# Optimization experiments

Hardware: AMD Instinct MI355X
Metric: run time of the kernel (lower is better)

The kernel has to match this reference:

```python
import jax, jax.numpy as jnp
import numpy as np
import math

B, T, C, NH = 4, 2048, 1024, 16
HS = C // NH  # 64

def rope_cache(dim, max_pos):
    half = dim // 2
    inv_freq = 1.0 / (10000.0 ** (jnp.arange(half, dtype=jnp.float32) * 2.0 / dim))
    ang = jnp.arange(max_pos, dtype=jnp.float32)[:, None] * inv_freq[None, :]
    return jnp.cos(ang), jnp.sin(ang)  # each [T, half]

def apply_rope(x, cos, sin):
    # x: [B, nH, T, hs]; rotate consecutive pairs (complex multiply)
    x0 = x[..., 0::2]
    x1 = x[..., 1::2]
    c = cos[None, None, :, :]
    s = sin[None, None, :, :]
    r0 = x0 * c - x1 * s
    r1 = x0 * s + x1 * c
    return jnp.stack([r0, r1], axis=-1).reshape(x.shape)

def setup_inputs() -> dict:
    key = jax.random.key(0)
    ks = jax.random.split(key, 5)
    sc = 1.0 / math.sqrt(C)
    return {
        "x": jax.random.normal(ks[0], (B, T, C), jnp.float32),
        "Wq": jax.random.normal(ks[1], (C, C), jnp.float32) * sc,
        "bq": jnp.zeros((C,), jnp.float32),
        "Wk": jax.random.normal(ks[2], (C, C), jnp.float32) * sc,
        "bk": jnp.zeros((C,), jnp.float32),
        "Wv": jax.random.normal(ks[3], (C, C), jnp.float32) * sc,
        "bv": jnp.zeros((C,), jnp.float32),
        "Wp": jax.random.normal(ks[4], (C, C), jnp.float32) * sc,
        "bp": jnp.zeros((C,), jnp.float32),
    }

def reference(x, Wq, bq, Wk, bk, Wv, bv, Wp, bp):
    Bx, Tx, Cx = x.shape
    def split_heads(y):
        return y.reshape(Bx, Tx, NH, HS).transpose(0, 2, 1, 3)  # [B,nH,T,hs]
    q = split_heads(x @ Wq + bq)
    k = split_heads(x @ Wk + bk)
    v = split_heads(x @ Wv + bv)
    cos, sin = rope_cache(HS, Tx)
    q = apply_rope(q, cos, sin)
    k = apply_rope(k, cos, sin)
    att = jnp.einsum("bhqd,bhkd->bhqk", q, k) * (1.0 / math.sqrt(HS))
    causal = jnp.tril(jnp.ones((Tx, Tx), bool))
    att = jnp.where(causal[None, None, :, :], att, jnp.float32(-1e10))
    att = jax.nn.softmax(att, axis=-1)
    y = jnp.einsum("bhqk,bhkd->bhqd", att, v)
    y = y.transpose(0, 2, 1, 3).reshape(Bx, Tx, Cx)
    return y @ Wp + bp
```

## Files before the change

kernel.cpp:

```cpp
#include <hip/hip_runtime.h>
#include <math.h>

#define B_  4
#define T_  2048
#define C_  1024
#define NH_ 16
#define HS_ 64
#define M_  (B_ * T_)
#define BH_ (B_ * NH_)

typedef __bf16 bf16_t;
typedef __bf16 bf16x8 __attribute__((ext_vector_type(8)));
typedef float  f32x4  __attribute__((ext_vector_type(4)));

__device__ __forceinline__ f32x4 mfma16(bf16x8 a, bf16x8 b, f32x4 c) {
    return __builtin_amdgcn_mfma_f32_16x16x32_bf16(a, b, c, 0, 0, 0);
}

#define GLOAD16(gp, lp) __builtin_amdgcn_global_load_lds( \
    (const __attribute__((address_space(1))) void*)(gp),  \
    (__attribute__((address_space(3))) void*)(lp), 16, 0, 0)


__global__ void cvt_x(const float* __restrict__ x, bf16_t* __restrict__ xb) {
    int i = blockIdx.x * blockDim.x + threadIdx.x;
    const float4* src = reinterpret_cast<const float4*>(x);
    float4 u = src[2 * i], v = src[2 * i + 1];
    bf16x8 o;
    o[0] = (bf16_t)u.x; o[1] = (bf16_t)u.y; o[2] = (bf16_t)u.z; o[3] = (bf16_t)u.w;
    o[4] = (bf16_t)v.x; o[5] = (bf16_t)v.y; o[6] = (bf16_t)v.z; o[7] = (bf16_t)v.w;
    *reinterpret_cast<bf16x8*>(xb + (size_t)i * 8) = o;
}

__global__ void wtrans(const float* __restrict__ W, bf16_t* __restrict__ Wt) {
    __shared__ float tile[32][33];
    int bx = blockIdx.x, by = blockIdx.y;
    int tx = threadIdx.x, ty = threadIdx.y;
    #pragma unroll
    for (int j = 0; j < 4; ++j)
        tile[ty + j * 8][tx] = W[(size_t)(by * 32 + ty + j * 8) * 1024 + bx * 32 + tx];
    __syncthreads();
    #pragma unroll
    for (int j = 0; j < 4; ++j)
        Wt[(size_t)(bx * 32 + ty + j * 8) * 1024 + by * 32 + tx] = (bf16_t)tile[tx][ty + j * 8];
}

__global__ void rope_tab(float* __restrict__ cs, float* __restrict__ sn) {
    int idx = blockIdx.x * blockDim.x + threadIdx.x;
    int t = idx >> 5, j = idx & 31;
    float inv = 1.0f / powf(10000.0f, ((float)(2 * j)) / 64.0f);
    float ang = (float)t * inv;
    cs[idx] = cosf(ang);
    sn[idx] = sinf(ang);
}

__global__ __launch_bounds__(512) void gemm_qkv(
    const bf16_t* __restrict__ A, const bf16_t* __restrict__ Bt,
    const float* __restrict__ bq, const float* __restrict__ bk, const float* __restrict__ bv,
    bf16_t* __restrict__ outq, bf16_t* __restrict__ outk, bf16_t* __restrict__ outvt) {
    __shared__ __align__(16) bf16_t Ab[2][256 * 64];
    __shared__ __align__(16) bf16_t Bb[2][128 * 64];
    int tid = threadIdx.x;
    int lane = tid & 63, w = tid >> 6;
    int rr = lane & 15, g = lane >> 4;
    int lin = blockIdx.y * 24 + blockIdx.x;
    int swz = (lin & 7) * 96 + (lin >> 3);
    int bx = swz % 24, by = swz / 24;
    int mbase = by * 256, nbase = bx * 128;
    int wm = (w >> 1) * 64, wn = (w & 1) * 64;
    int rA = tid >> 3;
    int cS = (tid & 7) ^ (rA & 7);
    const bf16_t* Asrc = A + (size_t)(mbase + rA) * 1024 + cS * 8;
    const bf16_t* Bsrc = Bt + (size_t)(nbase + rA) * 1024 + cS * 8;
    int r7 = rr & 7;
    int ch0 = ((0 + g) ^ r7) * 8, ch1 = ((4 + g) ^ r7) * 8;
    f32x4 acc[4][4] = {};

    #pragma unroll
    for (int j = 0; j < 4; ++j) GLOAD16(Asrc + (size_t)j * 64 * 1024, &Ab[0][tid * 8 + j * 4096]);
    #pragma unroll
    for (int j = 0; j < 2; ++j) GLOAD16(Bsrc + (size_t)j * 64 * 1024, &Bb[0][tid * 8 + j * 4096]);
    __syncthreads();
    int cur = 0;
    for (int t = 0; t < 16; ++t) {
        if (t < 15) {
            int kk = (t + 1) * 64;
            #pragma unroll
            for (int j = 0; j < 4; ++j) GLOAD16(Asrc + kk + (size_t)j * 64 * 1024, &Ab[cur ^ 1][tid * 8 + j * 4096]);
            #pragma unroll
            for (int j = 0; j < 2; ++j) GLOAD16(Bsrc + kk + (size_t)j * 64 * 1024, &Bb[cur ^ 1][tid * 8 + j * 4096]);
        }
        #pragma unroll
        for (int kk = 0; kk < 2; ++kk) {
            int co = kk ? ch1 : ch0;
            bf16x8 a[4], b[4];
            #pragma unroll
            for (int i = 0; i < 4; ++i) {
                a[i] = *(const bf16x8*)&Ab[cur][(wm + i * 16 + rr) * 64 + co];
                b[i] = *(const bf16x8*)&Bb[cur][(wn + i * 16 + rr) * 64 + co];
            }
            #pragma unroll
            for (int mi = 0; mi < 4; ++mi)
                #pragma unroll
                for (int ni = 0; ni < 4; ++ni)
                    acc[mi][ni] = mfma16(a[mi], b[ni], acc[mi][ni]);
        }
        __syncthreads();
        cur ^= 1;
    }
    #pragma unroll
    for (int ni = 0; ni < 4; ++ni) {
        int n = nbase + wn + ni * 16 + rr;
        int sel = n >> 10, nn = n & 1023, h = nn >> 6, d = nn & 63;
        float bias = (sel == 0) ? bq[nn] : (sel == 1) ? bk[nn] : bv[nn];
        #pragma unroll
        for (int mi = 0; mi < 4; ++mi) {
            #pragma unroll
            for (int j = 0; j < 4; ++j) {
                int mrow = mbase + wm + mi * 16 + g * 4 + j;
                int bI = mrow >> 11, t = mrow & 2047;
                float val = acc[mi][ni][j] + bias;
                size_t bh = (size_t)(bI * 16 + h);
                if (sel == 0)      outq[(bh * 2048 + t) * 64 + d] = (bf16_t)val;
                else if (sel == 1) outk[(bh * 2048 + t) * 64 + d] = (bf16_t)val;
                else               outvt[(bh * 64 + d) * 2048 + t] = (bf16_t)val;
            }
        }
    }
}

__global__ void rope_qk(bf16_t* __restrict__ q, bf16_t* __restrict__ k,
                        const float* __restrict__ cs, const float* __restrict__ sn) {
    int idx = blockIdx.x * blockDim.x + threadIdx.x;
    int seg = idx & 7;
    int t = (idx >> 3) & 2047;
    int bh = idx >> 14;
    float4 cc = *reinterpret_cast<const float4*>(cs + (t << 5) + seg * 4);
    float4 ss = *reinterpret_cast<const float4*>(sn + (t << 5) + seg * 4);
    size_t base = (((size_t)bh << 11) + t) * 64 + seg * 8;
    {
        bf16x8 v = *reinterpret_cast<bf16x8*>(q + base);
        bf16x8 o;
        o[0] = (bf16_t)((float)v[0] * cc.x - (float)v[1] * ss.x);
        o[1] = (bf16_t)((float)v[0] * ss.x + (float)v[1] * cc.x);
        o[2] = (bf16_t)((float)v[2] * cc.y - (float)v[3] * ss.y);
        o[3] = (bf16_t)((float)v[2] * ss.y + (float)v[3] * cc.y);
        o[4] = (bf16_t)((float)v[4] * cc.z - (float)v[5] * ss.z);
        o[5] = (bf16_t)((float)v[4] * ss.z + (float)v[5] * cc.z);
        o[6] = (bf16_t)((float)v[6] * cc.w - (float)v[7] * ss.w);
        o[7] = (bf16_t)((float)v[6] * ss.w + (float)v[7] * cc.w);
        *reinterpret_cast<bf16x8*>(q + base) = o;
    }
    {
        bf16x8 v = *reinterpret_cast<bf16x8*>(k + base);
        bf16x8 o;
        o[0] = (bf16_t)((float)v[0] * cc.x - (float)v[1] * ss.x);
        o[1] = (bf16_t)((float)v[0] * ss.x + (float)v[1] * cc.x);
        o[2] = (bf16_t)((float)v[2] * cc.y - (float)v[3] * ss.y);
        o[3] = (bf16_t)((float)v[2] * ss.y + (float)v[3] * cc.y);
        o[4] = (bf16_t)((float)v[4] * cc.z - (float)v[5] * ss.z);
        o[5] = (bf16_t)((float)v[4] * ss.z + (float)v[5] * cc.z);
        o[6] = (bf16_t)((float)v[6] * cc.w - (float)v[7] * ss.w);
        o[7] = (bf16_t)((float)v[6] * ss.w + (float)v[7] * cc.w);
        *reinterpret_cast<bf16x8*>(k + base) = o;
    }
}

__global__ __launch_bounds__(256) void attn(
    const bf16_t* __restrict__ q, const bf16_t* __restrict__ k,
    const bf16_t* __restrict__ vt, bf16_t* __restrict__ y) {
    __shared__ __align__(16) bf16_t Kb[2][64 * 64];
    __shared__ __align__(16) bf16_t Vb[2][64 * 64];
    int tid = threadIdx.x;
    int lane = tid & 63, w = tid >> 6;
    int rr = lane & 15, g = lane >> 4;
    int bid = blockIdx.x;
    int xcd = bid & 7, idx = bid >> 3;
    int bh = xcd * 8 + (idx >> 4);
    int xp = idx & 15;
    const bf16_t* qh = q + (size_t)bh * T_ * HS_;
    const bf16_t* kh = k + (size_t)bh * T_ * HS_;
    const bf16_t* vh = vt + (size_t)bh * HS_ * T_;
    int bI = bh >> 4, h = bh & 15;
    int s0 = ((rr >> 2) << 3) + (rr & 3);
    const float SC = 0.125f * 1.44269504088896f;

    int i2a = tid, i2b = tid + 256;
    int rwa = i2a >> 3, rwb = i2b >> 3;
    int swKa = (rwa & 3) | (((rwa >> 3) & 1) << 2);
    int swKb = (rwb & 3) | (((rwb >> 3) & 1) << 2);
    int cKa = (i2a & 7) ^ swKa, cKb = (i2b & 7) ^ swKb;
    int cVa = (i2a & 7) ^ (rwa & 7), cVb = (i2b & 7) ^ (rwb & 7);

    #pragma unroll 1
    for (int pass = 0; pass < 2; ++pass) {
        int qt = pass ? (31 - xp) : xp;
        int qbase = qt * 64;
        int qrow = qbase + w * 16 + rr;
        bf16x8 qf0 = *reinterpret_cast<const bf16x8*>(qh + (size_t)qrow * 64 + g * 8);
        bf16x8 qf1 = *reinterpret_cast<const bf16x8*>(qh + (size_t)qrow * 64 + 32 + g * 8);
        float mrun = -1e30f, lsum = 0.f;
        f32x4 oacc[4] = {};
        int nt = qt + 1;
        GLOAD16(kh + (size_t)rwa * 64 + cKa * 8, &Kb[0][i2a * 8]);
        GLOAD16(kh + (size_t)rwb * 64 + cKb * 8, &Kb[0][i2b * 8]);
        GLOAD16(vh + (size_t)rwa * 2048 + cVa * 8, &Vb[0][i2a * 8]);
        GLOAD16(vh + (size_t)rwb * 2048 + cVb * 8, &Vb[0][i2b * 8]);
        __syncthreads();
        int cur = 0;
        #pragma unroll 1
        for (int t = 0; t < nt; ++t) {
            if (t + 1 < nt) {
                int kv1 = (t + 1) * 64;
                GLOAD16(kh + (size_t)(kv1 + rwa) * 64 + cKa * 8, &Kb[cur ^ 1][i2a * 8]);
                GLOAD16(kh + (size_t)(kv1 + rwb) * 64 + cKb * 8, &Kb[cur ^ 1][i2b * 8]);
                GLOAD16(vh + (size_t)rwa * 2048 + kv1 + cVa * 8, &Vb[cur ^ 1][i2a * 8]);
                GLOAD16(vh + (size_t)rwb * 2048 + kv1 + cVb * 8, &Vb[cur ^ 1][i2b * 8]);
            }
            int kv0 = t * 64;
            f32x4 st[4] = {};
            #pragma unroll
            for (int s = 0; s < 2; ++s) {
                #pragma unroll
                for (int p = 0; p < 2; ++p) {
                    int row = s * 32 + s0 + p * 4;
                    int sw = (row & 3) | (((row >> 3) & 1) << 2);
                    bf16x8 k0 = *(const bf16x8*)&Kb[cur][row * 64 + ((g ^ sw) * 8)];
                    bf16x8 k1 = *(const bf16x8*)&Kb[cur][row * 64 + (((4 + g) ^ sw) * 8)];
                    st[2 * s + p] = mfma16(k0, qf0, st[2 * s + p]);
                    st[2 * s + p] = mfma16(k1, qf1, st[2 * s + p]);
                }
            }
            float sv[16];
            #pragma unroll
            for (int s = 0; s < 2; ++s)
                #pragma unroll
                for (int p = 0; p < 2; ++p)
                    #pragma unroll
                    for (int j = 0; j < 4; ++j)
                        sv[s * 8 + p * 4 + j] = st[2 * s + p][j] * SC;
            if (t == nt - 1) {
                #pragma unroll
                for (int i = 0; i < 16; ++i) {
                    int kvi = kv0 + (i >> 3) * 32 + g * 8 + (i & 7);
                    if (kvi > qrow) sv[i] = -1e30f;
                }
            }
            float pmax = sv[0];
            #pragma unroll
            for (int i = 1; i < 16; ++i) pmax = fmaxf(pmax, sv[i]);
            pmax = fmaxf(pmax, __shfl_xor(pmax, 16));
            pmax = fmaxf(pmax, __shfl_xor(pmax, 32));
            float mnew = fmaxf(mrun, pmax);
            float fac = __builtin_amdgcn_exp2f(mrun - mnew);
            float psum = 0.f;
            bf16x8 pf0, pf1;
            #pragma unroll
            for (int i = 0; i < 8; ++i) {
                float pe = __builtin_amdgcn_exp2f(sv[i] - mnew);
                psum += pe;
                pf0[i] = (bf16_t)pe;
            }
            #pragma unroll
            for (int i = 0; i < 8; ++i) {
                float pe = __builtin_amdgcn_exp2f(sv[8 + i] - mnew);
                psum += pe;
                pf1[i] = (bf16_t)pe;
            }
            psum += __shfl_xor(psum, 16);
            psum += __shfl_xor(psum, 32);
            lsum = lsum * fac + psum;
            mrun = mnew;
            #pragma unroll
            for (int ch = 0; ch < 4; ++ch) {
                #pragma unroll
                for (int j = 0; j < 4; ++j) oacc[ch][j] *= fac;
            }
            #pragma unroll
            for (int ch = 0; ch < 4; ++ch) {
                int row = ch * 16 + rr;
                bf16x8 v0 = *(const bf16x8*)&Vb[cur][row * 64 + ((g ^ (row & 7)) * 8)];
                bf16x8 v1 = *(const bf16x8*)&Vb[cur][row * 64 + (((4 + g) ^ (row & 7)) * 8)];
                oacc[ch] = mfma16(v0, pf0, oacc[ch]);
                oacc[ch] = mfma16(v1, pf1, oacc[ch]);
            }
            __syncthreads();
            cur ^= 1;
        }
        float inv = 1.0f / lsum;
        bf16_t* yrow = y + ((size_t)bI * 2048 + qrow) * 1024 + h * 64;
        #pragma unroll
        for (int ch = 0; ch < 4; ++ch) {
            union { bf16_t b[4]; short4 s4; } u;
            #pragma unroll
            for (int j = 0; j < 4; ++j) u.b[j] = (bf16_t)(oacc[ch][j] * inv);
            *reinterpret_cast<short4*>(yrow + ch * 16 + g * 4) = u.s4;
        }
    }
}

__global__ __launch_bounds__(512) void gemm_proj(
    const bf16_t* __restrict__ A, const bf16_t* __restrict__ Bt,
    const float* __restrict__ bp, float* __restrict__ out) {
    __shared__ __align__(16) bf16_t Ab[2][256 * 64];
    __shared__ __align__(16) bf16_t Bb[2][128 * 64];
    int tid = threadIdx.x;
    int lane = tid & 63, w = tid >> 6;
    int rr = lane & 15, g = lane >> 4;
    int lin = blockIdx.y * 8 + blockIdx.x;
    int swz = (lin & 7) * 32 + (lin >> 3);
    int bx = swz % 8, by = swz / 8;
    int mbase = by * 256, nbase = bx * 128;
    int wm = (w >> 1) * 64, wn = (w & 1) * 64;
    int rA = tid >> 3;
    int cS = (tid & 7) ^ (rA & 7);
    const bf16_t* Asrc = A + (size_t)(mbase + rA) * 1024 + cS * 8;
    const bf16_t* Bsrc = Bt + (size_t)(nbase + rA) * 1024 + cS * 8;
    int r7 = rr & 7;
    int ch0 = ((0 + g) ^ r7) * 8, ch1 = ((4 + g) ^ r7) * 8;
    f32x4 acc[4][4] = {};

    #pragma unroll
    for (int j = 0; j < 4; ++j) GLOAD16(Asrc + (size_t)j * 64 * 1024, &Ab[0][tid * 8 + j * 4096]);
    #pragma unroll
    for (int j = 0; j < 2; ++j) GLOAD16(Bsrc + (size_t)j * 64 * 1024, &Bb[0][tid * 8 + j * 4096]);
    __syncthreads();
    int cur = 0;
    for (int t = 0; t < 16; ++t) {
        if (t < 15) {
            int kk = (t + 1) * 64;
            #pragma unroll
            for (int j = 0; j < 4; ++j) GLOAD16(Asrc + kk + (size_t)j * 64 * 1024, &Ab[cur ^ 1][tid * 8 + j * 4096]);
            #pragma unroll
            for (int j = 0; j < 2; ++j) GLOAD16(Bsrc + kk + (size_t)j * 64 * 1024, &Bb[cur ^ 1][tid * 8 + j * 4096]);
        }
        #pragma unroll
        for (int kk = 0; kk < 2; ++kk) {
            int co = kk ? ch1 : ch0;
            bf16x8 a[4], b[4];
            #pragma unroll
            for (int i = 0; i < 4; ++i) {
                a[i] = *(const bf16x8*)&Ab[cur][(wm + i * 16 + rr) * 64 + co];
                b[i] = *(const bf16x8*)&Bb[cur][(wn + i * 16 + rr) * 64 + co];
            }
            #pragma unroll
            for (int mi = 0; mi < 4; ++mi)
                #pragma unroll
                for (int ni = 0; ni < 4; ++ni)
                    acc[mi][ni] = mfma16(a[mi], b[ni], acc[mi][ni]);
        }
        __syncthreads();
        cur ^= 1;
    }
    #pragma unroll
    for (int ni = 0; ni < 4; ++ni) {
        int n = nbase + wn + ni * 16 + rr;
        float bias = bp[n];
        #pragma unroll
        for (int mi = 0; mi < 4; ++mi) {
            #pragma unroll
            for (int j = 0; j < 4; ++j) {
                int mrow = mbase + wm + mi * 16 + g * 4 + j;
                out[(size_t)mrow * 1024 + n] = acc[mi][ni][j] + bias;
            }
        }
    }
}

extern "C" void kernel_launch(void* const* d_in, const int* in_sizes, int n_in,
                              void* d_out, int out_size, void* d_ws, size_t ws_size,
                              hipStream_t stream) {
    const float* x  = (const float*)d_in[0];
    const float* Wq = (const float*)d_in[1];
    const float* bq = (const float*)d_in[2];
    const float* Wk = (const float*)d_in[3];
    const float* bk = (const float*)d_in[4];
    const float* Wv = (const float*)d_in[5];
    const float* bv = (const float*)d_in[6];
    const float* Wp = (const float*)d_in[7];
    const float* bp = (const float*)d_in[8];
    float* out = (float*)d_out;

    char* p = (char*)d_ws;
    auto alloc = [&](size_t n) { char* r = p; p += (n + 255) & ~(size_t)255; return r; };
    bf16_t* xb    = (bf16_t*)alloc((size_t)M_ * C_ * 2);
    bf16_t* wtqkv = (bf16_t*)alloc((size_t)3 * C_ * C_ * 2);
    bf16_t* wtp   = (bf16_t*)alloc((size_t)C_ * C_ * 2);
    bf16_t* qb    = (bf16_t*)alloc((size_t)BH_ * T_ * HS_ * 2);
    bf16_t* kb    = (bf16_t*)alloc((size_t)BH_ * T_ * HS_ * 2);
    bf16_t* vtb   = (bf16_t*)alloc((size_t)BH_ * HS_ * T_ * 2);
    bf16_t* yb    = (bf16_t*)alloc((size_t)M_ * C_ * 2);
    float*  cs    = (float*)alloc((size_t)T_ * 32 * 4);
    float*  sn    = (float*)alloc((size_t)T_ * 32 * 4);

    cvt_x<<<4096, 256, 0, stream>>>(x, xb);
    wtrans<<<dim3(32, 32), dim3(32, 8), 0, stream>>>(Wq, wtqkv);
    wtrans<<<dim3(32, 32), dim3(32, 8), 0, stream>>>(Wk, wtqkv + (size_t)C_ * C_);
    wtrans<<<dim3(32, 32), dim3(32, 8), 0, stream>>>(Wv, wtqkv + (size_t)2 * C_ * C_);
    wtrans<<<dim3(32, 32), dim3(32, 8), 0, stream>>>(Wp, wtp);
    rope_tab<<<256, 256, 0, stream>>>(cs, sn);

    gemm_qkv<<<dim3(24, 32), 512, 0, stream>>>(xb, wtqkv, bq, bk, bv, qb, kb, vtb);
    rope_qk<<<4096, 256, 0, stream>>>(qb, kb, cs, sn);
    attn<<<1024, 256, 0, stream>>>(qb, kb, vtb, yb);
    gemm_proj<<<dim3(8, 32), 512, 0, stream>>>(yb, wtp, bp, out);
}
```

Baseline: 318.7 us.

## Triple-buffer GEMM mainloop with interleaved prefetch, barriers and MFMA priority

Both projection GEMMs now share one core that uses a three-stage LDS ring, so global-to-LDS copies run two k-tiles ahead. Each k-tile is split into four row-slices of MFMAs, and the prefetch loads, explicit vmcnt/lgkmcnt waits and barriers are interleaved between them. s_setprio is raised around each MFMA group to keep the matrix units fed while loads are issued. In exchange, LDS use grows to about 144KB per block and there are many more barriers. The launch bound of 2 blocks per CU also caps registers, which risks spills.

```diff
diff --git a/kernel.cpp b/kernel.cpp
--- a/kernel.cpp
+++ b/kernel.cpp
@@ -20,6 +20,14 @@
 #define GLOAD16(gp, lp) __builtin_amdgcn_global_load_lds( \
     (const __attribute__((address_space(1))) void*)(gp),  \
     (__attribute__((address_space(3))) void*)(lp), 16, 0, 0)
+
+#define SBAR() do { asm volatile("" ::: "memory"); \
+                    __builtin_amdgcn_s_barrier(); \
+                    __builtin_amdgcn_sched_barrier(0); } while (0)
+#define LGKM0() do { asm volatile("s_waitcnt lgkmcnt(0)" ::: "memory"); \
+                     __builtin_amdgcn_sched_barrier(0); } while (0)
+#define VMCNT6() do { asm volatile("s_waitcnt vmcnt(6)" ::: "memory"); \
+                      __builtin_amdgcn_sched_barrier(0); } while (0)
 
 
 __global__ void cvt_x(const float* __restrict__ x, bf16_t* __restrict__ xb) {
@@ -54,60 +62,122 @@
     sn[idx] = sinf(ang);
 }
 
-__global__ __launch_bounds__(512) void gemm_qkv(
-    const bf16_t* __restrict__ A, const bf16_t* __restrict__ Bt,
+__device__ __forceinline__ void gemm8_core(
+    const bf16_t* __restrict__ Aptr, const bf16_t* __restrict__ Bptr,
+    int mbase, int nbase, f32x4 (&acc)[4][4]) {
+    __shared__ __align__(16) bf16_t Ab[3][256 * 64];
+    __shared__ __align__(16) bf16_t Bb[3][128 * 64];
+    int tid = threadIdx.x;
+    int lane = tid & 63, w = tid >> 6;
+    int rr = lane & 15, g = lane >> 4, r7 = rr & 7;
+    int wm = (w >> 1) * 64, wn = (w & 1) * 64;
+    int rA = tid >> 3, cS = (tid & 7) ^ (rA & 7);
+    int dOff = rA * 64 + (tid & 7) * 8;
+    const bf16_t* As = Aptr + (size_t)(mbase + rA) * 1024 + cS * 8;
+    const bf16_t* Bs = Bptr + (size_t)(nbase + rA) * 1024 + cS * 8;
+    int co0 = (g ^ r7) * 8, co1 = ((4 + g) ^ r7) * 8;
+
+    GLOAD16(As,                   Ab[0] + dOff);
+    GLOAD16(As + 64 * 1024,       Ab[0] + 4096 + dOff);
+    GLOAD16(As + 128 * 1024,      Ab[0] + 8192 + dOff);
+    GLOAD16(As + 192 * 1024,      Ab[0] + 12288 + dOff);
+    GLOAD16(Bs,                   Bb[0] + dOff);
+    GLOAD16(Bs + 64 * 1024,       Bb[0] + 4096 + dOff);
+    GLOAD16(As + 64,              Ab[1] + dOff);
+    GLOAD16(As + 64 + 64 * 1024,  Ab[1] + 4096 + dOff);
+    GLOAD16(As + 64 + 128 * 1024, Ab[1] + 8192 + dOff);
+    GLOAD16(As + 64 + 192 * 1024, Ab[1] + 12288 + dOff);
+    GLOAD16(Bs + 64,              Bb[1] + dOff);
+    GLOAD16(Bs + 64 + 64 * 1024,  Bb[1] + 4096 + dOff);
+    VMCNT6();
+    SBAR();
+
+    int c = 0;
+    #pragma unroll 1
+    for (int t = 0; t < 16; ++t) {
+        bf16_t* pAc = Ab[c];
+        bf16_t* pBc = Bb[c];
+        int c2 = c + 2; if (c2 >= 3) c2 -= 3;
+        bf16_t* pAn = Ab[c2];
+        bf16_t* pBn = Bb[c2];
+        int k2 = (t + 2 < 16) ? (t + 2) : 15;
+        const bf16_t* As2 = As + k2 * 64;
+        const bf16_t* Bs2 = Bs + k2 * 64;
+        bf16x8 bfr[4][2], av0, av1;
+
+        #pragma unroll
+        for (int ni = 0; ni < 4; ++ni) {
+            bfr[ni][0] = *(const bf16x8*)&pBc[(wn + ni * 16 + rr) * 64 + co0];
+            bfr[ni][1] = *(const bf16x8*)&pBc[(wn + ni * 16 + rr) * 64 + co1];
+        }
+        av0 = *(const bf16x8*)&pAc[(wm + rr) * 64 + co0];
+        av1 = *(const bf16x8*)&pAc[(wm + rr) * 64 + co1];
+        GLOAD16(As2,             pAn + dOff);
+        GLOAD16(As2 + 64 * 1024, pAn + 4096 + dOff);
+        SBAR(); LGKM0();
+        __builtin_amdgcn_s_setprio(1);
+        #pragma unroll
+        for (int ni = 0; ni < 4; ++ni) acc[0][ni] = mfma16(av0, bfr[ni][0], acc[0][ni]);
+        #pragma unroll
+        for (int ni = 0; ni < 4; ++ni) acc[0][ni] = mfma16(av1, bfr[ni][1], acc[0][ni]);
+        __builtin_amdgcn_s_setprio(0);
+        SBAR();
+
+        av0 = *(const bf16x8*)&pAc[(wm + 16 + rr) * 64 + co0];
+        av1 = *(const bf16x8*)&pAc[(wm + 16 + rr) * 64 + co1];
+        GLOAD16(As2 + 128 * 1024, pAn + 8192 + dOff);
+        GLOAD16(As2 + 192 * 1024, pAn + 12288 + dOff);
+        SBAR(); LGKM0();
+        __builtin_amdgcn_s_setprio(1);
+        #pragma unroll
+        for (int ni = 0; ni < 4; ++ni) acc[1][ni] = mfma16(av0, bfr[ni][0], acc[1][ni]);
+        #pragma unroll
+        for (int ni = 0; ni < 4; ++ni) acc[1][ni] = mfma16(av1, bfr[ni][1], acc[1][ni]);
+        __builtin_amdgcn_s_setprio(0);
+        SBAR();
+
+        av0 = *(const bf16x8*)&pAc[(wm + 32 + rr) * 64 + co0];
+        av1 = *(const bf16x8*)&pAc[(wm + 32 + rr) * 64 + co1];
+        GLOAD16(Bs2, pBn + dOff);
+        SBAR(); LGKM0();
+        __builtin_amdgcn_s_setprio(1);
+        #pragma unroll
+        for (int ni = 0; ni < 4; ++ni) acc[2][ni] = mfma16(av0, bfr[ni][0], acc[2][ni]);
+        #pragma unroll
+        for (int ni = 0; ni < 4; ++ni) acc[2][ni] = mfma16(av1, bfr[ni][1], acc[2][ni]);
+        __builtin_amdgcn_s_setprio(0);
+        SBAR();
+
+        av0 = *(const bf16x8*)&pAc[(wm + 48 + rr) * 64 + co0];
+        av1 = *(const bf16x8*)&pAc[(wm + 48 + rr) * 64 + co1];
+        GLOAD16(Bs2 + 64 * 1024, pBn + 4096 + dOff);
+        VMCNT6();
+        SBAR(); LGKM0();
+        __builtin_amdgcn_s_setprio(1);
+        #pragma unroll
+        for (int ni = 0; ni < 4; ++ni) acc[3][ni] = mfma16(av0, bfr[ni][0], acc[3][ni]);
+        #pragma unroll
+        for (int ni = 0; ni < 4; ++ni) acc[3][ni] = mfma16(av1, bfr[ni][1], acc[3][ni]);
+        __builtin_amdgcn_s_setprio(0);
+        SBAR();
+
+        c = (c + 1 == 3) ? 0 : c + 1;
+    }
+}
+
+__global__ __launch_bounds__(512, 2) void gemm_qkv(
+    const bf16_t* __restrict__ Aptr, const bf16_t* __restrict__ Bptr,
     const float* __restrict__ bq, const float* __restrict__ bk, const float* __restrict__ bv,
     bf16_t* __restrict__ outq, bf16_t* __restrict__ outk, bf16_t* __restrict__ outvt) {
-    __shared__ __align__(16) bf16_t Ab[2][256 * 64];
-    __shared__ __align__(16) bf16_t Bb[2][128 * 64];
-    int tid = threadIdx.x;
-    int lane = tid & 63, w = tid >> 6;
-    int rr = lane & 15, g = lane >> 4;
     int lin = blockIdx.y * 24 + blockIdx.x;
     int swz = (lin & 7) * 96 + (lin >> 3);
     int bx = swz % 24, by = swz / 24;
     int mbase = by * 256, nbase = bx * 128;
+    f32x4 acc[4][4] = {};
+    gemm8_core(Aptr, Bptr, mbase, nbase, acc);
+    int lane = threadIdx.x & 63, w = threadIdx.x >> 6;
+    int rr = lane & 15, g = lane >> 4;
     int wm = (w >> 1) * 64, wn = (w & 1) * 64;
-    int rA = tid >> 3;
-    int cS = (tid & 7) ^ (rA & 7);
-    const bf16_t* Asrc = A + (size_t)(mbase + rA) * 1024 + cS * 8;
-    const bf16_t* Bsrc = Bt + (size_t)(nbase + rA) * 1024 + cS * 8;
-    int r7 = rr & 7;
-    int ch0 = ((0 + g) ^ r7) * 8, ch1 = ((4 + g) ^ r7) * 8;
-    f32x4 acc[4][4] = {};
-
-    #pragma unroll
-    for (int j = 0; j < 4; ++j) GLOAD16(Asrc + (size_t)j * 64 * 1024, &Ab[0][tid * 8 + j * 4096]);
-    #pragma unroll
-    for (int j = 0; j < 2; ++j) GLOAD16(Bsrc + (size_t)j * 64 * 1024, &Bb[0][tid * 8 + j * 4096]);
-    __syncthreads();
-    int cur = 0;
-    for (int t = 0; t < 16; ++t) {
-        if (t < 15) {
-            int kk = (t + 1) * 64;
-            #pragma unroll
-            for (int j = 0; j < 4; ++j) GLOAD16(Asrc + kk + (size_t)j * 64 * 1024, &Ab[cur ^ 1][tid * 8 + j * 4096]);
-            #pragma unroll
-            for (int j = 0; j < 2; ++j) GLOAD16(Bsrc + kk + (size_t)j * 64 * 1024, &Bb[cur ^ 1][tid * 8 + j * 4096]);
-        }
-        #pragma unroll
-        for (int kk = 0; kk < 2; ++kk) {
-            int co = kk ? ch1 : ch0;
-            bf16x8 a[4], b[4];
-            #pragma unroll
-            for (int i = 0; i < 4; ++i) {
-                a[i] = *(const bf16x8*)&Ab[cur][(wm + i * 16 + rr) * 64 + co];
-                b[i] = *(const bf16x8*)&Bb[cur][(wn + i * 16 + rr) * 64 + co];
-            }
-            #pragma unroll
-            for (int mi = 0; mi < 4; ++mi)
-                #pragma unroll
-                for (int ni = 0; ni < 4; ++ni)
-                    acc[mi][ni] = mfma16(a[mi], b[ni], acc[mi][ni]);
-        }
-        __syncthreads();
-        cur ^= 1;
-    }
     #pragma unroll
     for (int ni = 0; ni < 4; ++ni) {
         int n = nbase + wn + ni * 16 + rr;
@@ -118,12 +188,39 @@
             #pragma unroll
             for (int j = 0; j < 4; ++j) {
                 int mrow = mbase + wm + mi * 16 + g * 4 + j;
-                int bI = mrow >> 11, t = mrow & 2047;
+                int bI = mrow >> 11, tt = mrow & 2047;
                 float val = acc[mi][ni][j] + bias;
                 size_t bh = (size_t)(bI * 16 + h);
-                if (sel == 0)      outq[(bh * 2048 + t) * 64 + d] = (bf16_t)val;
-                else if (sel == 1) outk[(bh * 2048 + t) * 64 + d] = (bf16_t)val;
-                else               outvt[(bh * 64 + d) * 2048 + t] = (bf16_t)val;
+                if (sel == 0)      outq[(bh * 2048 + tt) * 64 + d] = (bf16_t)val;
+                else if (sel == 1) outk[(bh * 2048 + tt) * 64 + d] = (bf16_t)val;
+                else               outvt[(bh * 64 + d) * 2048 + tt] = (bf16_t)val;
+            }
+        }
+    }
+}
+
+__global__ __launch_bounds__(512, 2) void gemm_proj(
+    const bf16_t* __restrict__ Aptr, const bf16_t* __restrict__ Bptr,
+    const float* __restrict__ bp, float* __restrict__ out) {
+    int lin = blockIdx.y * 8 + blockIdx.x;
+    int swz = (lin & 7) * 32 + (lin >> 3);
+    int bx = swz % 8, by = swz / 8;
+    int mbase = by * 256, nbase = bx * 128;
+    f32x4 acc[4][4] = {};
+    gemm8_core(Aptr, Bptr, mbase, nbase, acc);
+    int lane = threadIdx.x & 63, w = threadIdx.x >> 6;
+    int rr = lane & 15, g = lane >> 4;
+    int wm = (w >> 1) * 64, wn = (w & 1) * 64;
+    #pragma unroll
+    for (int ni = 0; ni < 4; ++ni) {
+        int n = nbase + wn + ni * 16 + rr;
+        float bias = bp[n];
+        #pragma unroll
+        for (int mi = 0; mi < 4; ++mi) {
+            #pragma unroll
+            for (int j = 0; j < 4; ++j) {
+                int mrow = mbase + wm + mi * 16 + g * 4 + j;
+                out[(size_t)mrow * 1024 + n] = acc[mi][ni][j] + bias;
             }
         }
     }
@@ -299,74 +396,6 @@
     }
 }
 
-__global__ __launch_bounds__(512) void gemm_proj(
-    const bf16_t* __restrict__ A, const bf16_t* __restrict__ Bt,
-    const float* __restrict__ bp, float* __restrict__ out) {
-    __shared__ __align__(16) bf16_t Ab[2][256 * 64];
-    __shared__ __align__(16) bf16_t Bb[2][128 * 64];
-    int tid = threadIdx.x;
-    int lane = tid & 63, w = tid >> 6;
-    int rr = lane & 15, g = lane >> 4;
-    int lin = blockIdx.y * 8 + blockIdx.x;
-    int swz = (lin & 7) * 32 + (lin >> 3);
-    int bx = swz % 8, by = swz / 8;
-    int mbase = by * 256, nbase = bx * 128;
-    int wm = (w >> 1) * 64, wn = (w & 1) * 64;
-    int rA = tid >> 3;
-    int cS = (tid & 7) ^ (rA & 7);
-    const bf16_t* Asrc = A + (size_t)(mbase + rA) * 1024 + cS * 8;
-    const bf16_t* Bsrc = Bt + (size_t)(nbase + rA) * 1024 + cS * 8;
-    int r7 = rr & 7;
-    int ch0 = ((0 + g) ^ r7) * 8, ch1 = ((4 + g) ^ r7) * 8;
-    f32x4 acc[4][4] = {};
-
-    #pragma unroll
-    for (int j = 0; j < 4; ++j) GLOAD16(Asrc + (size_t)j * 64 * 1024, &Ab[0][tid * 8 + j * 4096]);
-    #pragma unroll
-    for (int j = 0; j < 2; ++j) GLOAD16(Bsrc + (size_t)j * 64 * 1024, &Bb[0][tid * 8 + j * 4096]);
-    __syncthreads();
-    int cur = 0;
-    for (int t = 0; t < 16; ++t) {
-        if (t < 15) {
-            int kk = (t + 1) * 64;
-            #pragma unroll
-            for (int j = 0; j < 4; ++j) GLOAD16(Asrc + kk + (size_t)j * 64 * 1024, &Ab[cur ^ 1][tid * 8 + j * 4096]);
-            #pragma unroll
-            for (int j = 0; j < 2; ++j) GLOAD16(Bsrc + kk + (size_t)j * 64 * 1024, &Bb[cur ^ 1][tid * 8 + j * 4096]);
-        }
-        #pragma unroll
-        for (int kk = 0; kk < 2; ++kk) {
-            int co = kk ? ch1 : ch0;
-            bf16x8 a[4], b[4];
-            #pragma unroll
-            for (int i = 0; i < 4; ++i) {
-                a[i] = *(const bf16x8*)&Ab[cur][(wm + i * 16 + rr) * 64 + co];
-                b[i] = *(const bf16x8*)&Bb[cur][(wn + i * 16 + rr) * 64 + co];
-            }
-            #pragma unroll
-            for (int mi = 0; mi < 4; ++mi)
-                #pragma unroll
-                for (int ni = 0; ni < 4; ++ni)
-                    acc[mi][ni] = mfma16(a[mi], b[ni], acc[mi][ni]);
-        }
-        __syncthreads();
-        cur ^= 1;
-    }
-    #pragma unroll
-    for (int ni = 0; ni < 4; ++ni) {
-        int n = nbase + wn + ni * 16 + rr;
-        float bias = bp[n];
-        #pragma unroll
-        for (int mi = 0; mi < 4; ++mi) {
-            #pragma unroll
-            for (int j = 0; j < 4; ++j) {
-                int mrow = mbase + wm + mi * 16 + g * 4 + j;
-                out[(size_t)mrow * 1024 + n] = acc[mi][ni][j] + bias;
-            }
-        }
-    }
-}
-
 extern "C" void kernel_launch(void* const* d_in, const int* in_sizes, int n_in,
                               void* d_out, int out_size, void* d_ws, size_t ws_size,
                               hipStream_t stream) {
```

Result: no change. 321.9 us (+1.0%).
